# Performance work log

Measured on AMD Instinct MI355X. Metric: run time of the kernel, lower is better.

Reference implementation:

```python
import jax, jax.numpy as jnp
import numpy as np

N_NODES = 50000
N_EDGES = 800000
IN_FEATS = 64
HID_FEATS = 64


def _sage_conv(x, src, dst, W_self, W_neigh, b):
    # mean aggregation over in-neighbors (messages flow src -> dst)
    msg_sum = jax.ops.segment_sum(x[src], dst, num_segments=N_NODES)  # [N, d]
    deg = jax.ops.segment_sum(jnp.ones((src.shape[0],), x.dtype), dst,
                              num_segments=N_NODES)  # [N]
    h_neigh = msg_sum / jnp.maximum(deg, 1.0)[:, None]  # zero-degree nodes -> 0
    return x @ W_self + h_neigh @ W_neigh + b


def setup_inputs() -> dict:
    key = jax.random.key(0)
    ks = jax.random.split(key, 12)
    inputs = jax.random.normal(ks[0], (N_NODES, IN_FEATS), dtype=jnp.float32)
    src = jax.random.randint(ks[1], (N_EDGES,), 0, N_NODES, dtype=jnp.int32)
    dst = jax.random.randint(ks[2], (N_EDGES,), 0, N_NODES, dtype=jnp.int32)

    def glorot(k, shape):
        lim = float(np.sqrt(6.0 / (shape[0] + shape[1])))
        return jax.random.uniform(k, shape, jnp.float32, -lim, lim)

    return {
        "inputs": inputs, "src": src, "dst": dst,
        "W_self1": glorot(ks[3], (IN_FEATS, HID_FEATS)),
        "W_neigh1": glorot(ks[4], (IN_FEATS, HID_FEATS)),
        "b1": jnp.zeros((HID_FEATS,), jnp.float32),
        "W_self2": glorot(ks[5], (HID_FEATS, HID_FEATS)),
        "W_neigh2": glorot(ks[6], (HID_FEATS, HID_FEATS)),
        "b2": jnp.zeros((HID_FEATS,), jnp.float32),
        "W_self3": glorot(ks[7], (HID_FEATS, 1)),
        "W_neigh3": glorot(ks[8], (HID_FEATS, 1)),
        "b3": jnp.zeros((1,), jnp.float32),
    }


def reference(inputs, src, dst,
              W_self1, W_neigh1, b1,
              W_self2, W_neigh2, b2,
              W_self3, W_neigh3, b3):
    h = jax.nn.relu(_sage_conv(inputs, src, dst, W_self1, W_neigh1, b1))
    h = jax.nn.relu(_sage_conv(h, src, dst, W_self2, W_neigh2, b2))
    h = _sage_conv(h, src, dst, W_self3, W_neigh3, b3)
    return h  # [N_NODES, 1]
```

## Files before the change

kernel.cpp:

```cpp
#include <hip/hip_runtime.h>

#define N_NODES 50000
#define N_EDGES 800000
#define F 64
#define NTILES (N_NODES / 16)

#define BNODES 128
#define NB ((N_NODES + BNODES - 1) / BNODES)
#define BCAP 2560
#define EPB 3200
#define SCAT_BLOCKS (N_EDGES / EPB)
#define PREP_ELEMS (4 * F * F + N_NODES * 16)
#define PREP_BLOCKS ((PREP_ELEMS + 511) / 512)

typedef __attribute__((ext_vector_type(8))) short short8;
typedef __attribute__((ext_vector_type(4))) float f32x4;

union frag16 { uint4 u; short8 s; };


__device__ __forceinline__ float bflo(unsigned int u) {
    union { unsigned int i; float f; } c; c.i = u << 16; return c.f;
}
__device__ __forceinline__ float bfhi(unsigned int u) {
    union { unsigned int i; float f; } c; c.i = u & 0xFFFF0000u; return c.f;
}
__device__ __forceinline__ unsigned short f2bf(float f) {
    union { float f; unsigned int i; } c; c.f = f;
    unsigned int r = c.i + 0x7FFF + ((c.i >> 16) & 1);
    return (unsigned short)(r >> 16);
}


__global__ __launch_bounds__(512) void scatter_prep(
        const int* __restrict__ src, const int* __restrict__ dst,
        int* __restrict__ bcur, unsigned int* __restrict__ binned,
        const float* __restrict__ W0, const float* __restrict__ W1,
        const float* __restrict__ W2, const float* __restrict__ W3,
        unsigned short* __restrict__ Wt,
        const float4* __restrict__ xin, ushort4* __restrict__ xout) {
    if (blockIdx.x >= SCAT_BLOCKS) {
        int idx = (blockIdx.x - SCAT_BLOCKS) * 512 + threadIdx.x;
        if (idx < 4 * F * F) {
            int m = idx >> 12;
            int e = idx & 4095;
            int n = e >> 6, k = e & 63;
            const float* W = (m == 0) ? W0 : (m == 1) ? W1 : (m == 2) ? W2 : W3;
            Wt[m * F * F + n * F + k] = f2bf(W[k * F + n]);
            return;
        }
        int i = idx - 4 * F * F;
        if (i >= N_NODES * 16) return;
        float4 v = xin[i];
        ushort4 o;
        o.x = f2bf(v.x); o.y = f2bf(v.y); o.z = f2bf(v.z); o.w = f2bf(v.w);
        xout[i] = o;
        return;
    }

    __shared__ int lcnt[NB];
    __shared__ int scan[512];
    __shared__ int gbase[NB];
    __shared__ int lcur[NB];
    __shared__ unsigned int staged[EPB];
    int tid = threadIdx.x;
    int e0 = blockIdx.x * EPB;
    int e1 = min(N_EDGES, e0 + EPB);
    for (int i = tid; i < NB; i += 512) lcnt[i] = 0;
    __syncthreads();
    for (int i = e0 + tid; i < e1; i += 512)
        atomicAdd(&lcnt[dst[i] >> 7], 1);
    __syncthreads();
    int v = (tid < NB) ? lcnt[tid] : 0;
    scan[tid] = v;
    __syncthreads();
    for (int off = 1; off < 512; off <<= 1) {
        int t = (tid >= off) ? scan[tid - off] : 0;
        __syncthreads();
        scan[tid] += t;
        __syncthreads();
    }
    if (tid < NB) {
        int excl = scan[tid] - v;
        int resv = (v > 0) ? atomicAdd(&bcur[tid], v) : 0;
        gbase[tid] = tid * BCAP + resv - excl;
        lcur[tid] = excl;
    }
    __syncthreads();
    for (int i = e0 + tid; i < e1; i += 512) {
        int d = dst[i];
        int b = d >> 7;
        int dl = d & 127;
        int posl = atomicAdd(&lcur[b], 1);
        staged[posl] = (unsigned)src[i] | ((unsigned)dl << 16) | ((unsigned)b << 23);
    }
    __syncthreads();
    int cnt = e1 - e0;
    for (int i = tid; i < cnt; i += 512) {
        unsigned pk = staged[i];
        int b = pk >> 23;
        binned[gbase[b] + i] = pk;
    }
}


__global__ __launch_bounds__(256) void bucket_build(const unsigned int* __restrict__ binned,
                                                    const int* __restrict__ bcur,
                                                    int* __restrict__ row_beg,
                                                    unsigned short* __restrict__ degs,
                                                    unsigned short* __restrict__ csr16) {
    int b = blockIdx.x;
    int start = b * BCAP;
    int cnt = bcur[b];
    __shared__ int ncnt[BNODES];
    __shared__ int nofs[BNODES];
    __shared__ int ncur[BNODES];
    int tid = threadIdx.x;
    for (int i = tid; i < BNODES; i += 256) ncnt[i] = 0;
    __syncthreads();
    for (int i = tid; i < cnt; i += 256)
        atomicAdd(&ncnt[(binned[start + i] >> 16) & 127], 1);
    __syncthreads();
    if (tid < 128) nofs[tid] = ncnt[tid];
    __syncthreads();
    for (int off = 1; off < 128; off <<= 1) {
        int t = (tid >= off && tid < 128) ? nofs[tid - off] : 0;
        __syncthreads();
        if (tid < 128) nofs[tid] += t;
        __syncthreads();
    }
    if (tid < 128) {
        int excl = nofs[tid] - ncnt[tid];
        ncur[tid] = excl;
        int node = b * BNODES + tid;
        row_beg[node] = start + excl;
        degs[node] = (unsigned short)ncnt[tid];
    }
    __syncthreads();
    for (int i = tid; i < cnt; i += 256) {
        unsigned pk = binned[start + i];
        int dl = (pk >> 16) & 127;
        int pos = start + atomicAdd(&ncur[dl], 1);
        csr16[pos] = (unsigned short)(pk & 0xFFFF);
    }
}


__global__ __launch_bounds__(256) void aggregate_kernel(
        const uint4* __restrict__ xh8, const int* __restrict__ row_beg,
        const unsigned short* __restrict__ degs,
        const unsigned short* __restrict__ csr16, uint4* __restrict__ aggh8, int n_nodes) {
    int wave = threadIdx.x >> 6;
    int lane = threadIdx.x & 63;
    int node = blockIdx.x * 4 + wave;
    if (node >= n_nodes) return;
    int g   = lane >> 3;
    int sub = lane & 7;
    int beg = row_beg[node];
    int deg = degs[node];
    int end = beg + deg;
    float a0[8], a1[8];
    #pragma unroll
    for (int j = 0; j < 8; ++j) { a0[j] = 0.f; a1[j] = 0.f; }
    int i = beg + g;
    for (; i + 8 < end; i += 16) {
        int i0 = csr16[i];
        int i1 = csr16[i + 8];
        uint4 v0 = xh8[i0 * 8 + sub];
        uint4 v1 = xh8[i1 * 8 + sub];
        a0[0] += bflo(v0.x); a0[1] += bfhi(v0.x); a0[2] += bflo(v0.y); a0[3] += bfhi(v0.y);
        a0[4] += bflo(v0.z); a0[5] += bfhi(v0.z); a0[6] += bflo(v0.w); a0[7] += bfhi(v0.w);
        a1[0] += bflo(v1.x); a1[1] += bfhi(v1.x); a1[2] += bflo(v1.y); a1[3] += bfhi(v1.y);
        a1[4] += bflo(v1.z); a1[5] += bfhi(v1.z); a1[6] += bflo(v1.w); a1[7] += bfhi(v1.w);
    }
    if (i < end) {
        uint4 v0 = xh8[csr16[i] * 8 + sub];
        a0[0] += bflo(v0.x); a0[1] += bfhi(v0.x); a0[2] += bflo(v0.y); a0[3] += bfhi(v0.y);
        a0[4] += bflo(v0.z); a0[5] += bfhi(v0.z); a0[6] += bflo(v0.w); a0[7] += bfhi(v0.w);
    }
    float s[8];
    #pragma unroll
    for (int j = 0; j < 8; ++j) s[j] = a0[j] + a1[j];
    #pragma unroll
    for (int off = 8; off <= 32; off <<= 1)
        #pragma unroll
        for (int j = 0; j < 8; ++j)
            s[j] += __shfl_xor(s[j], off);
    if (g == 0) {
        float inv = (deg > 0) ? (1.0f / (float)deg) : 0.f;
        unsigned short o[8];
        #pragma unroll
        for (int j = 0; j < 8; ++j) o[j] = f2bf(s[j] * inv);
        uint4 pk;
        pk.x = (unsigned)o[0] | ((unsigned)o[1] << 16);
        pk.y = (unsigned)o[2] | ((unsigned)o[3] << 16);
        pk.z = (unsigned)o[4] | ((unsigned)o[5] << 16);
        pk.w = (unsigned)o[6] | ((unsigned)o[7] << 16);
        aggh8[node * 8 + sub] = pk;
    }
}


__global__ __launch_bounds__(256) void mfma_transform(
        const uint4* __restrict__ xh, const uint4* __restrict__ aggh,
        const uint4* __restrict__ Wst, const uint4* __restrict__ Wnt,
        const float* __restrict__ b,
        unsigned short* __restrict__ out_bf,
        const float* __restrict__ Ws3, const float* __restrict__ Wn3,
        float* __restrict__ pout, float* __restrict__ qout, int ntiles) {
    int wv   = threadIdx.x >> 6;
    int lane = threadIdx.x & 63;
    int tile = blockIdx.x * 4 + wv;
    if (tile >= ntiles) return;
    int lo = lane & 15, hi = lane >> 4;

    frag16 ws[2][4], wn[2][4];
    #pragma unroll
    for (int kt = 0; kt < 2; ++kt)
        #pragma unroll
        for (int jt = 0; jt < 4; ++jt) {
            int n = jt * 16 + lo;
            ws[kt][jt].u = Wst[n * 8 + kt * 4 + hi];
            wn[kt][jt].u = Wnt[n * 8 + kt * 4 + hi];
        }

    float bias_s[4];
    #pragma unroll
    for (int jt = 0; jt < 4; ++jt) bias_s[jt] = b[jt * 16 + lo];
    float w3n_s[4], w3s_s[4];
    if (pout) {
        #pragma unroll
        for (int jt = 0; jt < 4; ++jt) {
            w3n_s[jt] = Wn3[jt * 16 + lo];
            w3s_s[jt] = Ws3[jt * 16 + lo];
        }
    }

    int base = tile * 16;
    int node = base + lo;

    frag16 ax[2], aa[2];
    #pragma unroll
    for (int kt = 0; kt < 2; ++kt) {
        ax[kt].u = xh[node * 8 + kt * 4 + hi];
        aa[kt].u = aggh[node * 8 + kt * 4 + hi];
    }

    f32x4 acc[4];
    #pragma unroll
    for (int jt = 0; jt < 4; ++jt)
        acc[jt] = f32x4{bias_s[jt], bias_s[jt], bias_s[jt], bias_s[jt]};

    #pragma unroll
    for (int kt = 0; kt < 2; ++kt)
        #pragma unroll
        for (int jt = 0; jt < 4; ++jt) {
            acc[jt] = __builtin_amdgcn_mfma_f32_16x16x32_bf16(ax[kt].s, ws[kt][jt].s, acc[jt], 0, 0, 0);
            acc[jt] = __builtin_amdgcn_mfma_f32_16x16x32_bf16(aa[kt].s, wn[kt][jt].s, acc[jt], 0, 0, 0);
        }

    if (out_bf) {
        #pragma unroll
        for (int jt = 0; jt < 4; ++jt)
            #pragma unroll
            for (int r = 0; r < 4; ++r) {
                float h = fmaxf(acc[jt][r], 0.f);
                out_bf[(base + hi * 4 + r) * F + jt * 16 + lo] = f2bf(h);
            }
    } else {
        #pragma unroll
        for (int r = 0; r < 4; ++r) {
            float pr = 0.f, qr = 0.f;
            #pragma unroll
            for (int jt = 0; jt < 4; ++jt) {
                float h = fmaxf(acc[jt][r], 0.f);
                pr += h * w3n_s[jt];
                qr += h * w3s_s[jt];
            }
            #pragma unroll
            for (int off = 1; off < 16; off <<= 1) {
                pr += __shfl_xor(pr, off);
                qr += __shfl_xor(qr, off);
            }
            if (lo == 0) {
                pout[base + hi * 4 + r] = pr;
                qout[base + hi * 4 + r] = qr;
            }
        }
    }
}


__global__ __launch_bounds__(256) void final_kernel(
        const int* __restrict__ row_beg, const unsigned short* __restrict__ degs,
        const unsigned short* __restrict__ csr16,
        const float* __restrict__ p, const float* __restrict__ q,
        const float* __restrict__ b3, float* __restrict__ out, int n_nodes) {
    int grp = threadIdx.x >> 4;
    int ln  = threadIdx.x & 15;
    int node = blockIdx.x * 16 + grp;
    if (node >= n_nodes) return;
    int beg = row_beg[node];
    int deg = degs[node];
    int end = beg + deg;
    float s = 0.f;
    for (int i = beg + ln; i < end; i += 16) s += p[csr16[i]];
    #pragma unroll
    for (int off = 1; off < 16; off <<= 1) s += __shfl_xor(s, off);
    if (ln == 0) {
        float inv = (deg > 0) ? (1.0f / (float)deg) : 0.f;
        out[node] = q[node] + s * inv + b3[0];
    }
}


extern "C" void kernel_launch(void* const* d_in, const int* in_sizes, int n_in,
                              void* d_out, int out_size, void* d_ws, size_t ws_size,
                              hipStream_t stream) {
    const float* x   = (const float*)d_in[0];
    const int*   src = (const int*)d_in[1];
    const int*   dst = (const int*)d_in[2];
    const float* Ws1 = (const float*)d_in[3];
    const float* Wn1 = (const float*)d_in[4];
    const float* b1  = (const float*)d_in[5];
    const float* Ws2 = (const float*)d_in[6];
    const float* Wn2 = (const float*)d_in[7];
    const float* b2  = (const float*)d_in[8];
    const float* Ws3 = (const float*)d_in[9];
    const float* Wn3 = (const float*)d_in[10];
    const float* b3  = (const float*)d_in[11];
    float* out = (float*)d_out;

    char* ws = (char*)d_ws;
    size_t cur = 0;
    auto alloc = [&](size_t bytes) -> void* {
        void* p = ws + cur;
        cur += (bytes + 255) & ~(size_t)255;
        return p;
    };

    int*            bcur     = (int*)  alloc(NB * sizeof(int));
    unsigned int*   binned   = (unsigned int*)alloc((size_t)NB * BCAP * sizeof(unsigned int));
    int*            row_beg  = (int*)  alloc((size_t)(NB * BNODES) * sizeof(int));
    unsigned short* degs     = (unsigned short*)alloc((size_t)(NB * BNODES) * sizeof(unsigned short));
    unsigned short* csr16    = (unsigned short*)alloc((size_t)NB * BCAP * sizeof(unsigned short));
    unsigned short* xh       = (unsigned short*)alloc((size_t)N_NODES * F * 2);
    unsigned short* h1h      = (unsigned short*)alloc((size_t)N_NODES * F * 2);
    unsigned short* aggh     = (unsigned short*)alloc((size_t)N_NODES * F * 2);
    unsigned short* Wt       = (unsigned short*)alloc(4 * F * F * 2);
    float*          p        = (float*)alloc(N_NODES * sizeof(float));
    float*          q        = (float*)alloc(N_NODES * sizeof(float));

    unsigned short* Wst1 = Wt;
    unsigned short* Wnt1 = Wt + F * F;
    unsigned short* Wst2 = Wt + 2 * F * F;
    unsigned short* Wnt2 = Wt + 3 * F * F;

    (void)hipMemsetAsync(bcur, 0, NB * sizeof(int), stream);
    scatter_prep<<<SCAT_BLOCKS + PREP_BLOCKS, 512, 0, stream>>>(
        src, dst, bcur, binned,
        Ws1, Wn1, Ws2, Wn2, Wt, (const float4*)x, (ushort4*)xh);
    bucket_build<<<NB, 256, 0, stream>>>(binned, bcur, row_beg, degs, csr16);

    int agg_grid = (N_NODES + 3) / 4;
    int tf_grid  = (NTILES + 3) / 4;

    aggregate_kernel<<<agg_grid, 256, 0, stream>>>(
        (const uint4*)xh, row_beg, degs, csr16, (uint4*)aggh, N_NODES);
    mfma_transform<<<tf_grid, 256, 0, stream>>>(
        (const uint4*)xh, (const uint4*)aggh, (const uint4*)Wst1, (const uint4*)Wnt1,
        b1, h1h, nullptr, nullptr, nullptr, nullptr, NTILES);
    aggregate_kernel<<<agg_grid, 256, 0, stream>>>(
        (const uint4*)h1h, row_beg, degs, csr16, (uint4*)aggh, N_NODES);
    mfma_transform<<<tf_grid, 256, 0, stream>>>(
        (const uint4*)h1h, (const uint4*)aggh, (const uint4*)Wst2, (const uint4*)Wnt2,
        b2, nullptr, Ws3, Wn3, p, q, NTILES);
    final_kernel<<<(N_NODES + 15) / 16, 256, 0, stream>>>(
        row_beg, degs, csr16, p, q, b3, out, N_NODES);
}
```

Baseline: 178.7 us.

## Split bf16 feature tables into two 32-column halves for cache-friendly gathers

```diff
diff --git a/kernel.cpp b/kernel.cpp
--- a/kernel.cpp
+++ b/kernel.cpp
@@ -38,7 +38,8 @@
         const float* __restrict__ W0, const float* __restrict__ W1,
         const float* __restrict__ W2, const float* __restrict__ W3,
         unsigned short* __restrict__ Wt,
-        const float4* __restrict__ xin, ushort4* __restrict__ xout) {
+        const float4* __restrict__ xin,
+        ushort4* __restrict__ xlo, ushort4* __restrict__ xhi) {
     if (blockIdx.x >= SCAT_BLOCKS) {
         int idx = (blockIdx.x - SCAT_BLOCKS) * 512 + threadIdx.x;
         if (idx < 4 * F * F) {
@@ -54,7 +55,9 @@
         float4 v = xin[i];
         ushort4 o;
         o.x = f2bf(v.x); o.y = f2bf(v.y); o.z = f2bf(v.z); o.w = f2bf(v.w);
-        xout[i] = o;
+        int node = i >> 4, c = i & 15;
+        if (c < 8) xlo[node * 8 + c] = o;
+        else       xhi[node * 8 + (c - 8)] = o;
         return;
     }
 
@@ -147,65 +150,59 @@
 
 
 __global__ __launch_bounds__(256) void aggregate_kernel(
-        const uint4* __restrict__ xh8, const int* __restrict__ row_beg,
-        const unsigned short* __restrict__ degs,
-        const unsigned short* __restrict__ csr16, uint4* __restrict__ aggh8, int n_nodes) {
+        const uint4* __restrict__ xlo, const uint4* __restrict__ xhi,
+        const int* __restrict__ row_beg, const unsigned short* __restrict__ degs,
+        const unsigned short* __restrict__ csr16,
+        uint4* __restrict__ alo, uint4* __restrict__ ahi) {
     int wave = threadIdx.x >> 6;
     int lane = threadIdx.x & 63;
-    int node = blockIdx.x * 4 + wave;
-    if (node >= n_nodes) return;
-    int g   = lane >> 3;
-    int sub = lane & 7;
+    int task = blockIdx.x * 4 + wave;
+    if (task >= 2 * N_NODES) return;
+    int half = (task >= N_NODES);
+    int node = task - half * N_NODES;
+    const uint4* tbl = half ? xhi : xlo;
+    uint4* outt = half ? ahi : alo;
+
+    int g   = lane >> 2;
+    int sub = lane & 3;
     int beg = row_beg[node];
     int deg = degs[node];
     int end = beg + deg;
-    float a0[8], a1[8];
-    #pragma unroll
-    for (int j = 0; j < 8; ++j) { a0[j] = 0.f; a1[j] = 0.f; }
-    int i = beg + g;
-    for (; i + 8 < end; i += 16) {
+    float a[8];
+    #pragma unroll
+    for (int j = 0; j < 8; ++j) a[j] = 0.f;
+    for (int i = beg + g; i < end; i += 16) {
         int i0 = csr16[i];
-        int i1 = csr16[i + 8];
-        uint4 v0 = xh8[i0 * 8 + sub];
-        uint4 v1 = xh8[i1 * 8 + sub];
-        a0[0] += bflo(v0.x); a0[1] += bfhi(v0.x); a0[2] += bflo(v0.y); a0[3] += bfhi(v0.y);
-        a0[4] += bflo(v0.z); a0[5] += bfhi(v0.z); a0[6] += bflo(v0.w); a0[7] += bfhi(v0.w);
-        a1[0] += bflo(v1.x); a1[1] += bfhi(v1.x); a1[2] += bflo(v1.y); a1[3] += bfhi(v1.y);
-        a1[4] += bflo(v1.z); a1[5] += bfhi(v1.z); a1[6] += bflo(v1.w); a1[7] += bfhi(v1.w);
-    }
-    if (i < end) {
-        uint4 v0 = xh8[csr16[i] * 8 + sub];
-        a0[0] += bflo(v0.x); a0[1] += bfhi(v0.x); a0[2] += bflo(v0.y); a0[3] += bfhi(v0.y);
-        a0[4] += bflo(v0.z); a0[5] += bfhi(v0.z); a0[6] += bflo(v0.w); a0[7] += bfhi(v0.w);
-    }
-    float s[8];
-    #pragma unroll
-    for (int j = 0; j < 8; ++j) s[j] = a0[j] + a1[j];
-    #pragma unroll
-    for (int off = 8; off <= 32; off <<= 1)
+        uint4 v = tbl[i0 * 4 + sub];
+        a[0] += bflo(v.x); a[1] += bfhi(v.x); a[2] += bflo(v.y); a[3] += bfhi(v.y);
+        a[4] += bflo(v.z); a[5] += bfhi(v.z); a[6] += bflo(v.w); a[7] += bfhi(v.w);
+    }
+    #pragma unroll
+    for (int off = 4; off <= 32; off <<= 1)
         #pragma unroll
         for (int j = 0; j < 8; ++j)
-            s[j] += __shfl_xor(s[j], off);
+            a[j] += __shfl_xor(a[j], off);
     if (g == 0) {
         float inv = (deg > 0) ? (1.0f / (float)deg) : 0.f;
         unsigned short o[8];
         #pragma unroll
-        for (int j = 0; j < 8; ++j) o[j] = f2bf(s[j] * inv);
+        for (int j = 0; j < 8; ++j) o[j] = f2bf(a[j] * inv);
         uint4 pk;
         pk.x = (unsigned)o[0] | ((unsigned)o[1] << 16);
         pk.y = (unsigned)o[2] | ((unsigned)o[3] << 16);
         pk.z = (unsigned)o[4] | ((unsigned)o[5] << 16);
         pk.w = (unsigned)o[6] | ((unsigned)o[7] << 16);
-        aggh8[node * 8 + sub] = pk;
+        outt[node * 4 + sub] = pk;
     }
 }
 
 
 __global__ __launch_bounds__(256) void mfma_transform(
-        const uint4* __restrict__ xh, const uint4* __restrict__ aggh,
+        const uint4* __restrict__ xlo, const uint4* __restrict__ xhi,
+        const uint4* __restrict__ alo, const uint4* __restrict__ ahi,
         const uint4* __restrict__ Wst, const uint4* __restrict__ Wnt,
         const float* __restrict__ b,
-        unsigned short* __restrict__ out_bf,
+        unsigned short* __restrict__ out_lo, unsigned short* __restrict__ out_hi,
         const float* __restrict__ Ws3, const float* __restrict__ Wn3,
         float* __restrict__ pout, float* __restrict__ qout, int ntiles) {
     int wv   = threadIdx.x >> 6;
@@ -240,11 +237,10 @@
     int node = base + lo;
 
     frag16 ax[2], aa[2];
-    #pragma unroll
-    for (int kt = 0; kt < 2; ++kt) {
-        ax[kt].u = xh[node * 8 + kt * 4 + hi];
-        aa[kt].u = aggh[node * 8 + kt * 4 + hi];
-    }
+    ax[0].u = xlo[node * 4 + hi];
+    ax[1].u = xhi[node * 4 + hi];
+    aa[0].u = alo[node * 4 + hi];
+    aa[1].u = ahi[node * 4 + hi];
 
     f32x4 acc[4];
     #pragma unroll
@@ -259,14 +255,17 @@
             acc[jt] = __builtin_amdgcn_mfma_f32_16x16x32_bf16(aa[kt].s, wn[kt][jt].s, acc[jt], 0, 0, 0);
         }
 
-    if (out_bf) {
-        #pragma unroll
-        for (int jt = 0; jt < 4; ++jt)
+    if (out_lo) {
+        #pragma unroll
+        for (int jt = 0; jt < 4; ++jt) {
+            unsigned short* otbl = (jt < 2) ? out_lo : out_hi;
+            int col = (jt & 1) * 16 + lo;
             #pragma unroll
             for (int r = 0; r < 4; ++r) {
                 float h = fmaxf(acc[jt][r], 0.f);
-                out_bf[(base + hi * 4 + r) * F + jt * 16 + lo] = f2bf(h);
+                otbl[(base + hi * 4 + r) * 32 + col] = f2bf(h);
             }
+        }
     } else {
         #pragma unroll
         for (int r = 0; r < 4; ++r) {
@@ -339,14 +338,19 @@
         return p;
     };
 
+    const size_t HT = (size_t)N_NODES * 32 * 2;
+
     int*            bcur     = (int*)  alloc(NB * sizeof(int));
     unsigned int*   binned   = (unsigned int*)alloc((size_t)NB * BCAP * sizeof(unsigned int));
     int*            row_beg  = (int*)  alloc((size_t)(NB * BNODES) * sizeof(int));
     unsigned short* degs     = (unsigned short*)alloc((size_t)(NB * BNODES) * sizeof(unsigned short));
     unsigned short* csr16    = (unsigned short*)alloc((size_t)NB * BCAP * sizeof(unsigned short));
-    unsigned short* xh       = (unsigned short*)alloc((size_t)N_NODES * F * 2);
-    unsigned short* h1h      = (unsigned short*)alloc((size_t)N_NODES * F * 2);
-    unsigned short* aggh     = (unsigned short*)alloc((size_t)N_NODES * F * 2);
+    unsigned short* xlo      = (unsigned short*)alloc(HT);
+    unsigned short* xhi      = (unsigned short*)alloc(HT);
+    unsigned short* h1lo     = (unsigned short*)alloc(HT);
+    unsigned short* h1hi     = (unsigned short*)alloc(HT);
+    unsigned short* aglo     = (unsigned short*)alloc(HT);
+    unsigned short* aghi     = (unsigned short*)alloc(HT);
     unsigned short* Wt       = (unsigned short*)alloc(4 * F * F * 2);
     float*          p        = (float*)alloc(N_NODES * sizeof(float));
     float*          q        = (float*)alloc(N_NODES * sizeof(float));
@@ -359,22 +363,26 @@
     (void)hipMemsetAsync(bcur, 0, NB * sizeof(int), stream);
     scatter_prep<<<SCAT_BLOCKS + PREP_BLOCKS, 512, 0, stream>>>(
         src, dst, bcur, binned,
-        Ws1, Wn1, Ws2, Wn2, Wt, (const float4*)x, (ushort4*)xh);
+        Ws1, Wn1, Ws2, Wn2, Wt, (const float4*)x, (ushort4*)xlo, (ushort4*)xhi);
     bucket_build<<<NB, 256, 0, stream>>>(binned, bcur, row_beg, degs, csr16);
 
-    int agg_grid = (N_NODES + 3) / 4;
+    int agg_grid = (2 * N_NODES + 3) / 4;
     int tf_grid  = (NTILES + 3) / 4;
 
     aggregate_kernel<<<agg_grid, 256, 0, stream>>>(
-        (const uint4*)xh, row_beg, degs, csr16, (uint4*)aggh, N_NODES);
+        (const uint4*)xlo, (const uint4*)xhi, row_beg, degs, csr16,
+        (uint4*)aglo, (uint4*)aghi);
     mfma_transform<<<tf_grid, 256, 0, stream>>>(
-        (const uint4*)xh, (const uint4*)aggh, (const uint4*)Wst1, (const uint4*)Wnt1,
-        b1, h1h, nullptr, nullptr, nullptr, nullptr, NTILES);
+        (const uint4*)xlo, (const uint4*)xhi, (const uint4*)aglo, (const uint4*)aghi,
+        (const uint4*)Wst1, (const uint4*)Wnt1, b1,
+        h1lo, h1hi, nullptr, nullptr, nullptr, nullptr, NTILES);
     aggregate_kernel<<<agg_grid, 256, 0, stream>>>(
-        (const uint4*)h1h, row_beg, degs, csr16, (uint4*)aggh, N_NODES);
+        (const uint4*)h1lo, (const uint4*)h1hi, row_beg, degs, csr16,
+        (uint4*)aglo, (uint4*)aghi);
     mfma_transform<<<tf_grid, 256, 0, stream>>>(
-        (const uint4*)h1h, (const uint4*)aggh, (const uint4*)Wst2, (const uint4*)Wnt2,
-        b2, nullptr, Ws3, Wn3, p, q, NTILES);
+        (const uint4*)h1lo, (const uint4*)h1hi, (const uint4*)aglo, (const uint4*)aghi,
+        (const uint4*)Wst2, (const uint4*)Wnt2, b2,
+        nullptr, nullptr, Ws3, Wn3, p, q, NTILES);
     final_kernel<<<(N_NODES + 15) / 16, 256, 0, stream>>>(
         row_beg, degs, csr16, p, q, b3, out, N_NODES);
 }
```

Measured after the change: 212.2 us. 18.8% more time.
